# Kernel optimization log

Hardware: AMD Instinct MI355X
Metric: run time of the kernel (lower is better)

The kernel has to match this reference:

```python
import jax, jax.numpy as jnp
import numpy as np

N, E, D, H = 10000, 160000, 128, 4  # nodes, edges, node/edge dim, heads
HC = H * D  # 512, concat output dim of TransformerConv
LN_EPS = 1e-5


def setup_inputs() -> dict:
    key = jax.random.key(0)
    ks = jax.random.split(key, 16)
    s = 1.0 / np.sqrt(D)
    s2 = 1.0 / np.sqrt(HC)
    return {
        "x": jax.random.normal(ks[0], (N, D), jnp.float32),
        "edge_index": jax.random.randint(ks[1], (2, E), 0, N, jnp.int64),
        "edge_attr": jax.random.normal(ks[2], (E, D), jnp.float32),
        "Wq": jax.random.normal(ks[3], (D, HC), jnp.float32) * s,
        "bq": jnp.zeros((HC,), jnp.float32),
        "Wk": jax.random.normal(ks[4], (D, HC), jnp.float32) * s,
        "bk": jnp.zeros((HC,), jnp.float32),
        "Wv": jax.random.normal(ks[5], (D, HC), jnp.float32) * s,
        "bv": jnp.zeros((HC,), jnp.float32),
        "We": jax.random.normal(ks[6], (D, HC), jnp.float32) * s,
        "be": jnp.zeros((HC,), jnp.float32),
        "Wskip": jax.random.normal(ks[7], (D, HC), jnp.float32) * s,
        "bskip": jnp.zeros((HC,), jnp.float32),
        "ln_g": jnp.ones((HC,), jnp.float32),
        "ln_b": jnp.zeros((HC,), jnp.float32),
        "Wlin": jax.random.normal(ks[8], (HC, D), jnp.float32) * s2,
        "blin": jnp.zeros((D,), jnp.float32),
    }


def reference(x, edge_index, edge_attr, Wq, bq, Wk, bk, Wv, bv, We, be,
              Wskip, bskip, ln_g, ln_b, Wlin, blin):
    n = x.shape[0]
    src, dst = edge_index[0], edge_index[1]  # message flows src -> dst
    q = (x @ Wq + bq).reshape(n, H, D)
    k = (x @ Wk + bk).reshape(n, H, D)
    v = (x @ Wv + bv).reshape(n, H, D)
    e = (edge_attr @ We + be).reshape(-1, H, D)  # [E,H,D]

    kj = k[src] + e                                   # [E,H,D]
    alpha = jnp.einsum('ehd,ehd->eh', q[dst], kj) / np.sqrt(D)  # [E,H]
    # per-destination-node, per-head softmax over incoming edges
    amax = jax.ops.segment_max(alpha, dst, num_segments=n)      # [N,H]
    ex = jnp.exp(alpha - amax[dst])
    denom = jax.ops.segment_sum(ex, dst, num_segments=n)        # [N,H]
    attn = ex / denom[dst]                                      # [E,H]

    msg = (v[src] + e) * attn[:, :, None]                       # [E,H,D]
    agg = jax.ops.segment_sum(msg, dst, num_segments=n).reshape(n, HC)
    out = agg + (x @ Wskip + bskip)  # root/skip connection (concat heads)

    # LayerNorm over H*D
    mu = out.mean(-1, keepdims=True)
    var = ((out - mu) ** 2).mean(-1, keepdims=True)
    normed = (out - mu) * jax.lax.rsqrt(var + LN_EPS) * ln_g + ln_b

    lin = normed @ Wlin + blin
    return jax.nn.elu(lin + x)
```

## Files before the change

kernel.cpp:

```cpp
#include <hip/hip_runtime.h>
#include <math.h>


typedef short bf16x8 __attribute__((ext_vector_type(8)));
typedef unsigned short u16x8 __attribute__((ext_vector_type(8)));
typedef float f32x4 __attribute__((ext_vector_type(4)));
typedef float fv4 __attribute__((ext_vector_type(4)));
typedef float f32x2 __attribute__((ext_vector_type(2)));
typedef unsigned int u32x4 __attribute__((ext_vector_type(4)));

#define SCALE 0.08838834764831845f

__device__ inline unsigned short f2bf(float f) {
    union { float f; unsigned u; } v; v.f = f;
    unsigned r = (v.u + 0x7FFFu + ((v.u >> 16) & 1u)) >> 16;
    return (unsigned short)r;
}
__device__ inline float bf2f(unsigned short u) {
    union { unsigned u; float f; } v; v.u = ((unsigned)u) << 16; return v.f;
}
__device__ inline fv4 ntload4(const float* p) {
    return __builtin_nontemporal_load((const fv4*)p);
}
__device__ inline f32x2 bfpair2f(unsigned u) {
    union { unsigned u; float f; } lo, hi;
    lo.u = u << 16; hi.u = u & 0xffff0000u;
    f32x2 r; r[0] = lo.f; r[1] = hi.f; return r;
}

__global__ __launch_bounds__(256) void wqe_k(
    const float* __restrict__ Wq, const float* __restrict__ bq,
    const float* __restrict__ We,
    float* __restrict__ WqeT, float* __restrict__ bqe,
    int* __restrict__ deg, int n)
{
    const int b = blockIdx.x, t = threadIdx.x;
    if (b < 64) {
        const int mt = b & 3, ct = (b >> 2) & 3, h = b >> 4;
        const int m0 = mt * 32, c0 = ct * 32;
        __shared__ float aq[32][129];
        __shared__ float awe[32][129];
        for (int i = t; i < 32 * 32; i += 256) {
            int r = i >> 5, ch = i & 31;
            float4 v = *(const float4*)&Wq[(size_t)(m0 + r) * 512 + h * 128 + ch * 4];
            *(float4*)&aq[r][ch * 4] = v;
            float4 w = *(const float4*)&We[(size_t)(c0 + r) * 512 + h * 128 + ch * 4];
            *(float4*)&awe[r][ch * 4] = w;
        }
        __syncthreads();
        const int ty = t >> 4, tx = t & 15;
        float acc[2][2] = {};
        #pragma unroll 4
        for (int d = 0; d < 128; ++d) {
            float a0 = aq[ty * 2][d], a1 = aq[ty * 2 + 1][d];
            float b0 = awe[tx * 2][d], b1 = awe[tx * 2 + 1][d];
            acc[0][0] += a0 * b0; acc[0][1] += a0 * b1;
            acc[1][0] += a1 * b0; acc[1][1] += a1 * b1;
        }
        #pragma unroll
        for (int i = 0; i < 2; ++i)
            #pragma unroll
            for (int j = 0; j < 2; ++j)
                WqeT[(size_t)(m0 + ty * 2 + i) * 512 + h * 128 + c0 + tx * 2 + j] = acc[i][j] * SCALE;
    } else if (b == 64) {
        __shared__ float bqs[512];
        for (int i = t; i < 512; i += 256) bqs[i] = bq[i];
        __syncthreads();
        for (int hc = t; hc < 512; hc += 256) {
            const int h = hc >> 7, c = hc & 127;
            const float* we = &We[(size_t)c * 512 + h * 128];
            const float* bb = &bqs[h * 128];
            float s = 0.f;
            #pragma unroll 8
            for (int d = 0; d < 128; ++d) s += bb[d] * we[d];
            bqe[hc] = s * SCALE;
        }
    } else {
        int idx = (b - 65) * 256 + t;
        if (idx < n) deg[idx] = 0;
    }
}

__global__ __launch_bounds__(256) void prep_k(
    const float* __restrict__ x,
    const float* __restrict__ Wq, const float* __restrict__ bq,
    const float* __restrict__ Wk, const float* __restrict__ bk,
    const float* __restrict__ Wv, const float* __restrict__ bv,
    const float* __restrict__ Ws, const float* __restrict__ bs,
    const float* __restrict__ WqeT, const float* __restrict__ bqe,
    const float* __restrict__ We, const float* __restrict__ Wlin,
    unsigned short* __restrict__ x_bf, unsigned short* __restrict__ Wfrag,
    unsigned short* __restrict__ Wefrag, unsigned short* __restrict__ Wlfrag,
    float* __restrict__ bcat,
    const int* __restrict__ ei, int* __restrict__ deg, int E, int n, int nb1)
{
    const int b = blockIdx.x, t = threadIdx.x;
    if (b < nb1) {
        int i = (b * 256 + t) * 4;
        if (i < n * 128) {
            float4 v = *(const float4*)&x[i];
            unsigned short o[4] = { f2bf(v.x), f2bf(v.y), f2bf(v.z), f2bf(v.w) };
            *(uint2*)&x_bf[i] = *(uint2*)o;
        }
    } else if (b < nb1 + 160) {
        int g = (b - nb1) * 256 + t;
        int lane = g & 63, kt = (g >> 6) & 3, nt = g >> 8;
        int ncol = nt * 16 + (lane & 15);
        int k0 = kt * 32 + ((lane >> 4) << 3);
        const float* W; int c; float sc = 1.f;
        if      (ncol < 512)  { W = Wq;   c = ncol; sc = SCALE; }
        else if (ncol < 1024) { W = Wk;   c = ncol - 512; }
        else if (ncol < 1536) { W = Wv;   c = ncol - 1024; }
        else if (ncol < 2048) { W = Ws;   c = ncol - 1536; }
        else                  { W = WqeT; c = ncol - 2048; }
        unsigned short o[8];
        #pragma unroll
        for (int j = 0; j < 8; ++j) o[j] = f2bf(W[(size_t)(k0 + j) * 512 + c] * sc);
        *(uint4*)&Wfrag[(size_t)g * 8] = *(uint4*)o;
    } else if (b < nb1 + 192) {
        int g = (b - nb1 - 160) * 256 + t;
        int lane = g & 63, kt = (g >> 6) & 3, nt = g >> 8;
        int ncol = nt * 16 + (lane & 15);
        int k0 = kt * 32 + ((lane >> 4) << 3);
        unsigned short o[8];
        #pragma unroll
        for (int j = 0; j < 8; ++j) o[j] = f2bf(We[(size_t)(k0 + j) * 512 + ncol]);
        *(uint4*)&Wefrag[(size_t)g * 8] = *(uint4*)o;
    } else if (b < nb1 + 224) {
        int g = (b - nb1 - 192) * 256 + t;
        int lane = g & 63, kt = (g >> 6) & 15, nt = g >> 10;
        int ncol = nt * 16 + (lane & 15);
        int k0 = kt * 32 + ((lane >> 4) << 3);
        unsigned short o[8];
        #pragma unroll
        for (int j = 0; j < 8; ++j) o[j] = f2bf(Wlin[(size_t)(k0 + j) * 128 + ncol]);
        *(uint4*)&Wlfrag[(size_t)g * 8] = *(uint4*)o;
    } else if (b < nb1 + 234) {
        int c = (b - nb1 - 224) * 256 + t;
        if (c < 2560)
            bcat[c] = (c < 512) ? bq[c] * SCALE : (c < 1024) ? bk[c - 512]
                     : (c < 1536) ? bv[c - 1024] : (c < 2048) ? bs[c - 1536] : bqe[c - 2048];
    } else {
        int e = (b - nb1 - 234) * 256 + t;
        if (e < E) atomicAdd(&deg[ei[E + e]], 1);
    }
}

__global__ __launch_bounds__(1024) void scan_k(const int* __restrict__ deg,
                                               int* __restrict__ row_start,
                                               int* __restrict__ cursor, int n)
{
    __shared__ int part[1024];
    const int t = threadIdx.x;
    const int c0 = t * 16;
    int loc[16];
    int s = 0;
    #pragma unroll
    for (int i = 0; i < 16; ++i) {
        int idx = c0 + i;
        int dv = (idx < n) ? deg[idx] : 0;
        loc[i] = s; s += dv;
    }
    part[t] = s;
    __syncthreads();
    int incl = s;
    for (int off = 1; off < 1024; off <<= 1) {
        int other = (t >= off) ? part[t - off] : 0;
        __syncthreads();
        incl += other;
        part[t] = incl;
        __syncthreads();
    }
    const int base = incl - s;
    #pragma unroll
    for (int i = 0; i < 16; ++i) {
        int idx = c0 + i;
        if (idx < n) { row_start[idx] = base + loc[i]; cursor[idx] = base + loc[i]; }
    }
    if (t == 1023) row_start[n] = incl;
}

__global__ __launch_bounds__(256) void node_gemm_mfma(
    const unsigned short* __restrict__ x_bf, const unsigned short* __restrict__ Wfrag,
    const float* __restrict__ bcat, unsigned short* __restrict__ qs_bf,
    unsigned short* __restrict__ kvq,
    const int* __restrict__ ei, int* __restrict__ cursor, int2* __restrict__ csr,
    int E, int n)
{
    if (blockIdx.y == 40) {
        const int nth = gridDim.x * 256;
        for (int e = blockIdx.x * 256 + threadIdx.x; e < E; e += nth) {
            int dnode = ei[E + e];
            int p = atomicAdd(&cursor[dnode], 1);
            csr[p] = make_int2(e, ei[e]);
        }
        return;
    }
    __shared__ float tile[64][68];
    const int t = threadIdx.x, lane = t & 63, w = t >> 6;
    const int bm = blockIdx.x * 64;
    const int by = blockIdx.y;
    const int m0 = (w >> 1) * 32;
    const int n0 = (w & 1) * 32;
    const int lr = lane & 15, lk = (lane >> 4) << 3;
    f32x4 acc[2][2] = {};
    #pragma unroll
    for (int kt = 0; kt < 4; ++kt) {
        bf16x8 a[2], bf[2];
        #pragma unroll
        for (int mi = 0; mi < 2; ++mi) {
            int row = bm + m0 + mi * 16 + lr; row = row < n ? row : n - 1;
            a[mi] = *(const bf16x8*)&x_bf[(size_t)row * 128 + kt * 32 + lk];
        }
        #pragma unroll
        for (int ni = 0; ni < 2; ++ni) {
            int nt = (by * 64 + n0 + ni * 16) >> 4;
            bf[ni] = *(const bf16x8*)&Wfrag[(size_t)((nt * 4 + kt) * 64 + lane) * 8];
        }
        #pragma unroll
        for (int mi = 0; mi < 2; ++mi)
            #pragma unroll
            for (int ni = 0; ni < 2; ++ni)
                acc[mi][ni] = __builtin_amdgcn_mfma_f32_16x16x32_bf16(a[mi], bf[ni], acc[mi][ni], 0, 0, 0);
    }
    #pragma unroll
    for (int mi = 0; mi < 2; ++mi)
        #pragma unroll
        for (int j = 0; j < 4; ++j)
            #pragma unroll
            for (int ni = 0; ni < 2; ++ni)
                tile[m0 + mi * 16 + (lane >> 4) * 4 + j][n0 + ni * 16 + lr] = acc[mi][ni][j];
    __syncthreads();
    const int r = t >> 2, cs = (t & 3) * 16;
    const int row = bm + r;
    if (row < n) {
        const int colg0 = by * 64 + cs;
        unsigned short o[16];
        #pragma unroll
        for (int i = 0; i < 16; ++i) o[i] = f2bf(tile[r][cs + i] + bcat[colg0 + i]);
        unsigned short* dst;
        if (by < 24)      dst = &kvq[(size_t)row * 2048 + colg0];
        else if (by < 32) dst = &qs_bf[(size_t)row * 512 + (colg0 - 1536)];
        else              dst = &kvq[(size_t)row * 2048 + (colg0 - 512)];
        *(uint4*)dst = *(uint4*)o;
        *(uint4*)(dst + 8) = *(uint4*)&o[8];
    }
}

__global__ __launch_bounds__(256, 4) void edge_k(
    const unsigned short* __restrict__ kvq, const float* __restrict__ ea,
    const float* __restrict__ be,
    const int* __restrict__ row_start, const int2* __restrict__ csr,
    unsigned short* __restrict__ wsum_bf, unsigned short* __restrict__ vacc_bf, int n)
{
    const int t = threadIdx.x, lane = t & 63, w = t >> 6;
    const int slot = w >> 1, half = w & 1;
    const int node = blockIdx.x * 2 + slot;
    const bool nvalid = node < n;
    const int nodec = nvalid ? node : 0;
    const int g = lane >> 4;
    const int l15 = lane & 15;
    const int sl = l15 * 8;

    __shared__ float lds_m[2][4], lds_den[2][4];
    __shared__ float lds_va[2][4][128], lds_ws[2][4][128];

    int rs = 0, deg = 0;
    if (nvalid) { rs = row_start[node]; deg = row_start[node + 1] - rs; }
    const int dh = (deg + 1) >> 1;
    const int lo = half ? dh : 0;
    const int myc = half ? (deg - dh) : dh;

    f32x2 q2[4], qe2[4];
    {
        const u32x4 uq  = *(const u32x4*)&kvq[(size_t)nodec * 2048 + g * 128 + sl];
        const u32x4 uqe = *(const u32x4*)&kvq[(size_t)nodec * 2048 + 1536 + g * 128 + sl];
        #pragma unroll
        for (int j = 0; j < 4; ++j) { q2[j] = bfpair2f(uq[j]); qe2[j] = bfpair2f(uqe[j]); }
    }
    float qbe;
    {
        const f32x2* bp = (const f32x2*)&be[g * 128 + sl];
        f32x2 pb2 = q2[0] * bp[0] + q2[1] * bp[1] + q2[2] * bp[2] + q2[3] * bp[3];
        float pb = pb2[0] + pb2[1];
        #pragma unroll
        for (int o = 1; o <= 8; o <<= 1) pb += __shfl_xor(pb, o);
        qbe = pb;
    }

    float m = -3.0e38f, den = 0.f;
    f32x2 va2[4] = {}, ws2[4] = {};

    for (int j0 = 0; j0 < myc; j0 += 64) {
        const int cnt = min(64, myc - j0);
        int2 my = make_int2(0, 0);
        if (lane < cnt) my = csr[rs + lo + j0 + lane];

        fv4 cA0, cB0, cA1, cB1; u32x4 cK0, cV0, cK1, cV1;
        {
            const int i1 = (1 < cnt) ? 1 : 0;
            const int e0 = __shfl(my.x, 0), s0_ = __shfl(my.y, 0);
            const int e1 = __shfl(my.x, i1), s1_ = __shfl(my.y, i1);
            const float* ep0 = &ea[(size_t)e0 * 128 + sl];
            const float* ep1 = &ea[(size_t)e1 * 128 + sl];
            cA0 = ntload4(ep0); cB0 = ntload4(ep0 + 4);
            cA1 = ntload4(ep1); cB1 = ntload4(ep1 + 4);
            cK0 = *(const u32x4*)&kvq[(size_t)s0_ * 2048 + 512 + g * 128 + sl];
            cV0 = *(const u32x4*)&kvq[(size_t)s0_ * 2048 + 1024 + g * 128 + sl];
            cK1 = *(const u32x4*)&kvq[(size_t)s1_ * 2048 + 512 + g * 128 + sl];
            cV1 = *(const u32x4*)&kvq[(size_t)s1_ * 2048 + 1024 + g * 128 + sl];
        }

        for (int jj = 0; jj < cnt; jj += 2) {
            fv4 nA0, nB0, nA1, nB1; u32x4 nK0, nV0, nK1, nV1;
            {
                const int nj = (jj + 2 < cnt) ? jj + 2 : jj;
                const int i1 = (nj + 1 < cnt) ? nj + 1 : nj;
                const int e0 = __shfl(my.x, nj), s0_ = __shfl(my.y, nj);
                const int e1 = __shfl(my.x, i1), s1_ = __shfl(my.y, i1);
                const float* ep0 = &ea[(size_t)e0 * 128 + sl];
                const float* ep1 = &ea[(size_t)e1 * 128 + sl];
                nA0 = ntload4(ep0); nB0 = ntload4(ep0 + 4);
                nA1 = ntload4(ep1); nB1 = ntload4(ep1 + 4);
                nK0 = *(const u32x4*)&kvq[(size_t)s0_ * 2048 + 512 + g * 128 + sl];
                nV0 = *(const u32x4*)&kvq[(size_t)s0_ * 2048 + 1024 + g * 128 + sl];
                nK1 = *(const u32x4*)&kvq[(size_t)s1_ * 2048 + 512 + g * 128 + sl];
                nV1 = *(const u32x4*)&kvq[(size_t)s1_ * 2048 + 1024 + g * 128 + sl];
            }
            const bool two = (jj + 1 < cnt);
            f32x2 ef0[4], ef1[4], kf0[4], kf1[4];
            ef0[0][0]=cA0.x; ef0[0][1]=cA0.y; ef0[1][0]=cA0.z; ef0[1][1]=cA0.w;
            ef0[2][0]=cB0.x; ef0[2][1]=cB0.y; ef0[3][0]=cB0.z; ef0[3][1]=cB0.w;
            ef1[0][0]=cA1.x; ef1[0][1]=cA1.y; ef1[1][0]=cA1.z; ef1[1][1]=cA1.w;
            ef1[2][0]=cB1.x; ef1[2][1]=cB1.y; ef1[3][0]=cB1.z; ef1[3][1]=cB1.w;
            #pragma unroll
            for (int j = 0; j < 4; ++j) { kf0[j] = bfpair2f(cK0[j]); kf1[j] = bfpair2f(cK1[j]); }
            f32x2 acc0 = {0.f, 0.f}, acc1 = {0.f, 0.f};
            #pragma unroll
            for (int j = 0; j < 4; ++j) {
                acc0 += q2[j] * kf0[j] + qe2[j] * ef0[j];
                acc1 += q2[j] * kf1[j] + qe2[j] * ef1[j];
            }
            float p0 = acc0[0] + acc0[1];
            float p1 = acc1[0] + acc1[1];
            #pragma unroll
            for (int o = 1; o <= 8; o <<= 1) {
                p0 += __shfl_xor(p0, o);
                p1 += __shfl_xor(p1, o);
            }
            const float a0 = p0 + qbe;
            const float a1 = two ? (p1 + qbe) : -3.0e38f;
            const float gm = fmaxf(a0, a1);
            if (gm > m + 8.f) {
                const float sc = __expf(m - gm);
                den *= sc;
                #pragma unroll
                for (int j = 0; j < 4; ++j) { va2[j] *= sc; ws2[j] *= sc; }
                m = gm;
            }
            const float w0 = __expf(a0 - m);
            const float w1 = __expf(a1 - m);
            den += w0 + w1;
            #pragma unroll
            for (int j = 0; j < 4; ++j) {
                va2[j] += bfpair2f(cV0[j]) * w0 + bfpair2f(cV1[j]) * w1;
                ws2[j] += ef0[j] * w0 + ef1[j] * w1;
            }
            cA0 = nA0; cB0 = nB0; cA1 = nA1; cB1 = nB1;
            cK0 = nK0; cV0 = nV0; cK1 = nK1; cV1 = nV1;
        }
    }

    if (half == 1) {
        if (l15 == 0) { lds_m[slot][g] = m; lds_den[slot][g] = den; }
        #pragma unroll
        for (int j = 0; j < 4; ++j) {
            *(f32x2*)&lds_va[slot][g][sl + 2 * j] = va2[j];
            *(f32x2*)&lds_ws[slot][g][sl + 2 * j] = ws2[j];
        }
    }
    __syncthreads();
    if (half == 0 && nvalid) {
        const float m1 = lds_m[slot][g], den1 = lds_den[slot][g];
        const float M = fmaxf(m, m1);
        const float s0 = __expf(m - M), s1 = __expf(m1 - M);
        const float dtot = den * s0 + den1 * s1;
        const float rden = (dtot > 0.f) ? 1.f / dtot : 0.f;
        unsigned short vo[8], wo[8];
        #pragma unroll
        for (int j = 0; j < 4; ++j) {
            f32x2 ov = (va2[j] * s0 + *(const f32x2*)&lds_va[slot][g][sl + 2 * j] * s1) * rden;
            f32x2 ow = (ws2[j] * s0 + *(const f32x2*)&lds_ws[slot][g][sl + 2 * j] * s1) * rden;
            vo[2 * j] = f2bf(ov[0]); vo[2 * j + 1] = f2bf(ov[1]);
            wo[2 * j] = f2bf(ow[0]); wo[2 * j + 1] = f2bf(ow[1]);
        }
        *(uint4*)&vacc_bf[(size_t)node * 512 + g * 128 + sl] = *(uint4*)vo;
        *(uint4*)&wsum_bf[(size_t)node * 512 + g * 128 + sl] = *(uint4*)wo;
    }
}

__global__ __launch_bounds__(256) void tail_k(
    const unsigned short* __restrict__ wsum_bf, const unsigned short* __restrict__ Wefrag,
    const float* __restrict__ be, const unsigned short* __restrict__ vacc_bf,
    const unsigned short* __restrict__ qs_bf, const int* __restrict__ row_start,
    const unsigned short* __restrict__ Wlfrag, const float* __restrict__ lng,
    const float* __restrict__ lnb, const float* __restrict__ blin,
    const float* __restrict__ x, float* __restrict__ out, int n)
{
    const int t = threadIdx.x, lane = t & 63, w = t >> 6;
    const int r0 = blockIdx.x * 16;
    const int lr = lane & 15, lk = (lane >> 4) << 3;
    __shared__ unsigned short nlds[16][520];
    __shared__ float red_s[4][16], red_q[4][16], mval[16], rval[16];

    f32x4 acc[8] = {};
    #pragma unroll
    for (int kt = 0; kt < 4; ++kt) {
        int row = r0 + lr; row = row < n ? row : n - 1;
        bf16x8 a = *(const bf16x8*)&wsum_bf[(size_t)row * 512 + w * 128 + kt * 32 + lk];
        #pragma unroll
        for (int ni = 0; ni < 8; ++ni) {
            bf16x8 bfr = *(const bf16x8*)&Wefrag[(size_t)(((w * 8 + ni) * 4 + kt) * 64 + lane) * 8];
            acc[ni] = __builtin_amdgcn_mfma_f32_16x16x32_bf16(a, bfr, acc[ni], 0, 0, 0);
        }
    }
    float g8[8], b8[8];
    #pragma unroll
    for (int ni = 0; ni < 8; ++ni) { int col = w * 128 + ni * 16 + lr; g8[ni] = lng[col]; b8[ni] = lnb[col]; }
    float sum_[4], sq_[4];
    #pragma unroll
    for (int j = 0; j < 4; ++j) {
        int row = r0 + (lane >> 4) * 4 + j;
        int rowc = row < n ? row : n - 1;
        const float hb = (row_start[rowc + 1] > row_start[rowc]) ? 1.f : 0.f;
        float s = 0.f, q = 0.f;
        #pragma unroll
        for (int ni = 0; ni < 8; ++ni) {
            int col = w * 128 + ni * 16 + lr;
            float y = acc[ni][j] + bf2f(vacc_bf[(size_t)rowc * 512 + col]) + hb * be[col]
                    + bf2f(qs_bf[(size_t)rowc * 512 + col]);
            acc[ni][j] = y;
            s += y; q += y * y;
        }
        sum_[j] = s; sq_[j] = q;
    }
    #pragma unroll
    for (int o = 1; o <= 8; o <<= 1) {
        #pragma unroll
        for (int j = 0; j < 4; ++j) { sum_[j] += __shfl_xor(sum_[j], o); sq_[j] += __shfl_xor(sq_[j], o); }
    }
    if (lr == 0) {
        #pragma unroll
        for (int j = 0; j < 4; ++j) {
            red_s[w][(lane >> 4) * 4 + j] = sum_[j];
            red_q[w][(lane >> 4) * 4 + j] = sq_[j];
        }
    }
    __syncthreads();
    if (t < 16) {
        float S = red_s[0][t] + red_s[1][t] + red_s[2][t] + red_s[3][t];
        float Q = red_q[0][t] + red_q[1][t] + red_q[2][t] + red_q[3][t];
        float mu = S * (1.f / 512.f);
        float var = Q * (1.f / 512.f) - mu * mu;
        mval[t] = mu;
        rval[t] = rsqrtf(fmaxf(var, 0.f) + 1e-5f);
    }
    __syncthreads();
    #pragma unroll
    for (int j = 0; j < 4; ++j) {
        int rowl = (lane >> 4) * 4 + j;
        float mu = mval[rowl], rv = rval[rowl];
        #pragma unroll
        for (int ni = 0; ni < 8; ++ni) {
            int col = w * 128 + ni * 16 + lr;
            nlds[rowl][col] = f2bf((acc[ni][j] - mu) * rv * g8[ni] + b8[ni]);
        }
    }
    __syncthreads();
    f32x4 acc2[2] = {};
    #pragma unroll
    for (int kt = 0; kt < 16; ++kt) {
        bf16x8 a2 = *(const bf16x8*)&nlds[lr][kt * 32 + lk];
        #pragma unroll
        for (int ni = 0; ni < 2; ++ni) {
            bf16x8 bfr = *(const bf16x8*)&Wlfrag[(size_t)(((w * 2 + ni) * 16 + kt) * 64 + lane) * 8];
            acc2[ni] = __builtin_amdgcn_mfma_f32_16x16x32_bf16(a2, bfr, acc2[ni], 0, 0, 0);
        }
    }
    #pragma unroll
    for (int j = 0; j < 4; ++j) {
        int row = r0 + (lane >> 4) * 4 + j;
        if (row < n) {
            #pragma unroll
            for (int ni = 0; ni < 2; ++ni) {
                int col = w * 32 + ni * 16 + lr;
                float z = acc2[ni][j] + blin[col] + x[(size_t)row * 128 + col];
                out[(size_t)row * 128 + col] = z > 0.f ? z : expm1f(z);
            }
        }
    }
}

extern "C" void kernel_launch(void* const* d_in, const int* in_sizes, int n_in,
                              void* d_out, int out_size, void* d_ws, size_t ws_size,
                              hipStream_t stream)
{
    const float* x   = (const float*)d_in[0];
    const int*   ei  = (const int*)d_in[1];
    const float* ea  = (const float*)d_in[2];
    const float* Wq  = (const float*)d_in[3];
    const float* bq  = (const float*)d_in[4];
    const float* Wk  = (const float*)d_in[5];
    const float* bk  = (const float*)d_in[6];
    const float* Wv  = (const float*)d_in[7];
    const float* bv  = (const float*)d_in[8];
    const float* We  = (const float*)d_in[9];
    const float* be  = (const float*)d_in[10];
    const float* Wsk = (const float*)d_in[11];
    const float* bsk = (const float*)d_in[12];
    const float* lng = (const float*)d_in[13];
    const float* lnb = (const float*)d_in[14];
    const float* Wl  = (const float*)d_in[15];
    const float* bl  = (const float*)d_in[16];
    float* out = (float*)d_out;

    const int n = in_sizes[0] / 128;
    const int E = in_sizes[1] / 2;

    float* WqeT  = (float*)d_ws;
    float* bqe   = WqeT + 128 * 512;
    float* bcat  = bqe + 512;
    unsigned short* x_bf    = (unsigned short*)(bcat + 2560);
    unsigned short* qs_bf   = x_bf + (size_t)n * 128;
    unsigned short* wsum_bf = qs_bf + (size_t)n * 512;
    unsigned short* vacc_bf = wsum_bf + (size_t)n * 512;
    unsigned short* kvq     = vacc_bf + (size_t)n * 512;
    unsigned short* Wfrag   = kvq + (size_t)n * 2048;
    unsigned short* Wefrag  = Wfrag + 128 * 2560;
    unsigned short* Wlfrag  = Wefrag + 128 * 512;
    int2* csr = (int2*)(((uintptr_t)(Wlfrag + 512 * 128) + 7) & ~(uintptr_t)7);
    int* deg       = (int*)(csr + E);
    int* row_start = deg + n;
    int* cursor    = row_start + n + 1;

    const int ndegb = (n + 255) / 256;
    wqe_k<<<65 + ndegb, 256, 0, stream>>>(Wq, bq, We, WqeT, bqe, deg, n);
    const int nb1 = (n * 32 + 255) / 256;
    const int ndc = (E + 255) / 256;
    prep_k<<<nb1 + 234 + ndc, 256, 0, stream>>>(x, Wq, bq, Wk, bk, Wv, bv, Wsk, bsk, WqeT, bqe,
                                                We, Wl, x_bf, Wfrag, Wefrag, Wlfrag, bcat,
                                                ei, deg, E, n, nb1);
    scan_k<<<1, 1024, 0, stream>>>(deg, row_start, cursor, n);
    dim3 g1((n + 63) / 64, 41);
    node_gemm_mfma<<<g1, 256, 0, stream>>>(x_bf, Wfrag, bcat, qs_bf, kvq, ei, cursor, csr, E, n);
    edge_k<<<(n + 1) / 2, 256, 0, stream>>>(kvq, ea, be, row_start, csr,
                                            wsum_bf, vacc_bf, n);
    tail_k<<<(n + 15) / 16, 256, 0, stream>>>(wsum_bf, Wefrag, be, vacc_bf, qs_bf, row_start,
                                              Wlfrag, lng, lnb, bl, x, out, n);
}
```

Before: 170.0 us.

## Split each node's edges across four waves and fold Wqe precompute into prep

The edge kernel now runs one node per block and splits its incoming edges across four waves, merging partial softmax state (max, denominator, weighted sums) through LDS. Before, one block handled two nodes with two waves each. The separate wqe_k launch is removed: the Wq·We^T fragments and their bias are computed inline in prep_k, and the degree zeroing becomes a hipMemsetAsync. This cuts a kernel launch and raises edge-level parallelism for high-degree nodes. In exchange, prep threads recompute 128-length dot products per element, the reduction step does more LDS traffic, and twice as many edge blocks are launched.

Measured after the change: 205.8 us. +21.0%, slower.

```diff
diff --git a/kernel.cpp b/kernel.cpp
--- a/kernel.cpp
+++ b/kernel.cpp
@@ -28,66 +28,12 @@
     f32x2 r; r[0] = lo.f; r[1] = hi.f; return r;
 }
 
-__global__ __launch_bounds__(256) void wqe_k(
-    const float* __restrict__ Wq, const float* __restrict__ bq,
-    const float* __restrict__ We,
-    float* __restrict__ WqeT, float* __restrict__ bqe,
-    int* __restrict__ deg, int n)
-{
-    const int b = blockIdx.x, t = threadIdx.x;
-    if (b < 64) {
-        const int mt = b & 3, ct = (b >> 2) & 3, h = b >> 4;
-        const int m0 = mt * 32, c0 = ct * 32;
-        __shared__ float aq[32][129];
-        __shared__ float awe[32][129];
-        for (int i = t; i < 32 * 32; i += 256) {
-            int r = i >> 5, ch = i & 31;
-            float4 v = *(const float4*)&Wq[(size_t)(m0 + r) * 512 + h * 128 + ch * 4];
-            *(float4*)&aq[r][ch * 4] = v;
-            float4 w = *(const float4*)&We[(size_t)(c0 + r) * 512 + h * 128 + ch * 4];
-            *(float4*)&awe[r][ch * 4] = w;
-        }
-        __syncthreads();
-        const int ty = t >> 4, tx = t & 15;
-        float acc[2][2] = {};
-        #pragma unroll 4
-        for (int d = 0; d < 128; ++d) {
-            float a0 = aq[ty * 2][d], a1 = aq[ty * 2 + 1][d];
-            float b0 = awe[tx * 2][d], b1 = awe[tx * 2 + 1][d];
-            acc[0][0] += a0 * b0; acc[0][1] += a0 * b1;
-            acc[1][0] += a1 * b0; acc[1][1] += a1 * b1;
-        }
-        #pragma unroll
-        for (int i = 0; i < 2; ++i)
-            #pragma unroll
-            for (int j = 0; j < 2; ++j)
-                WqeT[(size_t)(m0 + ty * 2 + i) * 512 + h * 128 + c0 + tx * 2 + j] = acc[i][j] * SCALE;
-    } else if (b == 64) {
-        __shared__ float bqs[512];
-        for (int i = t; i < 512; i += 256) bqs[i] = bq[i];
-        __syncthreads();
-        for (int hc = t; hc < 512; hc += 256) {
-            const int h = hc >> 7, c = hc & 127;
-            const float* we = &We[(size_t)c * 512 + h * 128];
-            const float* bb = &bqs[h * 128];
-            float s = 0.f;
-            #pragma unroll 8
-            for (int d = 0; d < 128; ++d) s += bb[d] * we[d];
-            bqe[hc] = s * SCALE;
-        }
-    } else {
-        int idx = (b - 65) * 256 + t;
-        if (idx < n) deg[idx] = 0;
-    }
-}
-
 __global__ __launch_bounds__(256) void prep_k(
     const float* __restrict__ x,
     const float* __restrict__ Wq, const float* __restrict__ bq,
     const float* __restrict__ Wk, const float* __restrict__ bk,
     const float* __restrict__ Wv, const float* __restrict__ bv,
     const float* __restrict__ Ws, const float* __restrict__ bs,
-    const float* __restrict__ WqeT, const float* __restrict__ bqe,
     const float* __restrict__ We, const float* __restrict__ Wlin,
     unsigned short* __restrict__ x_bf, unsigned short* __restrict__ Wfrag,
     unsigned short* __restrict__ Wefrag, unsigned short* __restrict__ Wlfrag,
@@ -107,15 +53,27 @@
         int lane = g & 63, kt = (g >> 6) & 3, nt = g >> 8;
         int ncol = nt * 16 + (lane & 15);
         int k0 = kt * 32 + ((lane >> 4) << 3);
-        const float* W; int c; float sc = 1.f;
-        if      (ncol < 512)  { W = Wq;   c = ncol; sc = SCALE; }
-        else if (ncol < 1024) { W = Wk;   c = ncol - 512; }
-        else if (ncol < 1536) { W = Wv;   c = ncol - 1024; }
-        else if (ncol < 2048) { W = Ws;   c = ncol - 1536; }
-        else                  { W = WqeT; c = ncol - 2048; }
         unsigned short o[8];
-        #pragma unroll
-        for (int j = 0; j < 8; ++j) o[j] = f2bf(W[(size_t)(k0 + j) * 512 + c] * sc);
+        if (ncol < 2048) {
+            const float* W; int c; float sc = 1.f;
+            if      (ncol < 512)  { W = Wq; c = ncol; sc = SCALE; }
+            else if (ncol < 1024) { W = Wk; c = ncol - 512; }
+            else if (ncol < 1536) { W = Wv; c = ncol - 1024; }
+            else                  { W = Ws; c = ncol - 1536; }
+            #pragma unroll
+            for (int j = 0; j < 8; ++j) o[j] = f2bf(W[(size_t)(k0 + j) * 512 + c] * sc);
+        } else {
+            int hc = ncol - 2048, h = hc >> 7, c = hc & 127;
+            const float* we = &We[(size_t)c * 512 + h * 128];
+            #pragma unroll
+            for (int j = 0; j < 8; ++j) {
+                const float* wq = &Wq[(size_t)(k0 + j) * 512 + h * 128];
+                float s0 = 0.f, s1 = 0.f;
+                #pragma unroll 8
+                for (int d = 0; d < 128; d += 2) { s0 += wq[d] * we[d]; s1 += wq[d + 1] * we[d + 1]; }
+                o[j] = f2bf((s0 + s1) * SCALE);
+            }
+        }
         *(uint4*)&Wfrag[(size_t)g * 8] = *(uint4*)o;
     } else if (b < nb1 + 192) {
         int g = (b - nb1 - 160) * 256 + t;
@@ -137,9 +95,18 @@
         *(uint4*)&Wlfrag[(size_t)g * 8] = *(uint4*)o;
     } else if (b < nb1 + 234) {
         int c = (b - nb1 - 224) * 256 + t;
-        if (c < 2560)
+        if (c < 2048) {
             bcat[c] = (c < 512) ? bq[c] * SCALE : (c < 1024) ? bk[c - 512]
-                     : (c < 1536) ? bv[c - 1024] : (c < 2048) ? bs[c - 1536] : bqe[c - 2048];
+                     : (c < 1536) ? bv[c - 1024] : bs[c - 1536];
+        } else if (c < 2560) {
+            int hc = c - 2048, h = hc >> 7, cc = hc & 127;
+            const float* we = &We[(size_t)cc * 512 + h * 128];
+            const float* bb = &bq[h * 128];
+            float s = 0.f;
+            #pragma unroll 8
+            for (int d = 0; d < 128; ++d) s += bb[d] * we[d];
+            bcat[c] = s * SCALE;
+        }
     } else {
         int e = (b - nb1 - 234) * 256 + t;
         if (e < E) atomicAdd(&deg[ei[E + e]], 1);
@@ -254,27 +221,23 @@
     unsigned short* __restrict__ wsum_bf, unsigned short* __restrict__ vacc_bf, int n)
 {
     const int t = threadIdx.x, lane = t & 63, w = t >> 6;
-    const int slot = w >> 1, half = w & 1;
-    const int node = blockIdx.x * 2 + slot;
-    const bool nvalid = node < n;
-    const int nodec = nvalid ? node : 0;
+    const int node = blockIdx.x;
     const int g = lane >> 4;
     const int l15 = lane & 15;
     const int sl = l15 * 8;
 
-    __shared__ float lds_m[2][4], lds_den[2][4];
-    __shared__ float lds_va[2][4][128], lds_ws[2][4][128];
-
-    int rs = 0, deg = 0;
-    if (nvalid) { rs = row_start[node]; deg = row_start[node + 1] - rs; }
-    const int dh = (deg + 1) >> 1;
-    const int lo = half ? dh : 0;
-    const int myc = half ? (deg - dh) : dh;
+    __shared__ float lds_m[4][4], lds_den[4][4];
+    __shared__ float lds_va[4][4][128], lds_ws[4][4][128];
+
+    const int rs = row_start[node];
+    const int deg = row_start[node + 1] - rs;
+    const int lo = (deg * w) >> 2;
+    const int myc = ((deg * (w + 1)) >> 2) - lo;
 
     f32x2 q2[4], qe2[4];
     {
-        const u32x4 uq  = *(const u32x4*)&kvq[(size_t)nodec * 2048 + g * 128 + sl];
-        const u32x4 uqe = *(const u32x4*)&kvq[(size_t)nodec * 2048 + 1536 + g * 128 + sl];
+        const u32x4 uq  = *(const u32x4*)&kvq[(size_t)node * 2048 + g * 128 + sl];
+        const u32x4 uqe = *(const u32x4*)&kvq[(size_t)node * 2048 + 1536 + g * 128 + sl];
         #pragma unroll
         for (int j = 0; j < 4; ++j) { q2[j] = bfpair2f(uq[j]); qe2[j] = bfpair2f(uqe[j]); }
     }
@@ -371,26 +334,32 @@
         }
     }
 
-    if (half == 1) {
-        if (l15 == 0) { lds_m[slot][g] = m; lds_den[slot][g] = den; }
-        #pragma unroll
-        for (int j = 0; j < 4; ++j) {
-            *(f32x2*)&lds_va[slot][g][sl + 2 * j] = va2[j];
-            *(f32x2*)&lds_ws[slot][g][sl + 2 * j] = ws2[j];
-        }
+    if (l15 == 0) { lds_m[w][g] = m; lds_den[w][g] = den; }
+    #pragma unroll
+    for (int j = 0; j < 4; ++j) {
+        *(f32x2*)&lds_va[w][g][sl + 2 * j] = va2[j];
+        *(f32x2*)&lds_ws[w][g][sl + 2 * j] = ws2[j];
     }
     __syncthreads();
-    if (half == 0 && nvalid) {
-        const float m1 = lds_m[slot][g], den1 = lds_den[slot][g];
-        const float M = fmaxf(m, m1);
-        const float s0 = __expf(m - M), s1 = __expf(m1 - M);
-        const float dtot = den * s0 + den1 * s1;
+    if (w == 0) {
+        const float m0_ = lds_m[0][g], m1_ = lds_m[1][g], m2_ = lds_m[2][g], m3_ = lds_m[3][g];
+        const float M = fmaxf(fmaxf(m0_, m1_), fmaxf(m2_, m3_));
+        const float s0 = __expf(m0_ - M), s1 = __expf(m1_ - M);
+        const float s2 = __expf(m2_ - M), s3 = __expf(m3_ - M);
+        const float dtot = lds_den[0][g] * s0 + lds_den[1][g] * s1
+                         + lds_den[2][g] * s2 + lds_den[3][g] * s3;
         const float rden = (dtot > 0.f) ? 1.f / dtot : 0.f;
         unsigned short vo[8], wo[8];
         #pragma unroll
         for (int j = 0; j < 4; ++j) {
-            f32x2 ov = (va2[j] * s0 + *(const f32x2*)&lds_va[slot][g][sl + 2 * j] * s1) * rden;
-            f32x2 ow = (ws2[j] * s0 + *(const f32x2*)&lds_ws[slot][g][sl + 2 * j] * s1) * rden;
+            f32x2 ov = (*(const f32x2*)&lds_va[0][g][sl + 2 * j] * s0
+                      + *(const f32x2*)&lds_va[1][g][sl + 2 * j] * s1
+                      + *(const f32x2*)&lds_va[2][g][sl + 2 * j] * s2
+                      + *(const f32x2*)&lds_va[3][g][sl + 2 * j] * s3) * rden;
+            f32x2 ow = (*(const f32x2*)&lds_ws[0][g][sl + 2 * j] * s0
+                      + *(const f32x2*)&lds_ws[1][g][sl + 2 * j] * s1
+                      + *(const f32x2*)&lds_ws[2][g][sl + 2 * j] * s2
+                      + *(const f32x2*)&lds_ws[3][g][sl + 2 * j] * s3) * rden;
             vo[2 * j] = f2bf(ov[0]); vo[2 * j + 1] = f2bf(ov[1]);
             wo[2 * j] = f2bf(ow[0]); wo[2 * j + 1] = f2bf(ow[1]);
         }
@@ -527,9 +496,7 @@
     const int n = in_sizes[0] / 128;
     const int E = in_sizes[1] / 2;
 
-    float* WqeT  = (float*)d_ws;
-    float* bqe   = WqeT + 128 * 512;
-    float* bcat  = bqe + 512;
+    float* bcat  = (float*)d_ws;
     unsigned short* x_bf    = (unsigned short*)(bcat + 2560);
     unsigned short* qs_bf   = x_bf + (size_t)n * 128;
     unsigned short* wsum_bf = qs_bf + (size_t)n * 512;
@@ -543,18 +510,16 @@
     int* row_start = deg + n;
     int* cursor    = row_start + n + 1;
 
-    const int ndegb = (n + 255) / 256;
-    wqe_k<<<65 + ndegb, 256, 0, stream>>>(Wq, bq, We, WqeT, bqe, deg, n);
+    hipMemsetAsync(deg, 0, (size_t)n * sizeof(int), stream);
     const int nb1 = (n * 32 + 255) / 256;
     const int ndc = (E + 255) / 256;
-    prep_k<<<nb1 + 234 + ndc, 256, 0, stream>>>(x, Wq, bq, Wk, bk, Wv, bv, Wsk, bsk, WqeT, bqe,
+    prep_k<<<nb1 + 234 + ndc, 256, 0, stream>>>(x, Wq, bq, Wk, bk, Wv, bv, Wsk, bsk,
                                                 We, Wl, x_bf, Wfrag, Wefrag, Wlfrag, bcat,
                                                 ei, deg, E, n, nb1);
     scan_k<<<1, 1024, 0, stream>>>(deg, row_start, cursor, n);
     dim3 g1((n + 63) / 64, 41);
     node_gemm_mfma<<<g1, 256, 0, stream>>>(x_bf, Wfrag, bcat, qs_bf, kvq, ei, cursor, csr, E, n);
-    edge_k<<<(n + 1) / 2, 256, 0, stream>>>(kvq, ea, be, row_start, csr,
-                                            wsum_bf, vacc_bf, n);
+    edge_k<<<n, 256, 0, stream>>>(kvq, ea, be, row_start, csr, wsum_bf, vacc_bf, n);
     tail_k<<<(n + 15) / 16, 256, 0, stream>>>(wsum_bf, Wefrag, be, vacc_bf, qs_bf, row_start,
                                               Wlfrag, lng, lnb, bl, x, out, n);
 }
```
